# Kernel optimization log

Hardware: AMD Instinct MI355X
Metric: run time of the kernel (lower is better)

The kernel has to match this reference:

```python
import jax, jax.numpy as jnp
import numpy as np

K = 4096
D = 64
DECAY = 0.99
EPS = 1e-05


def setup_inputs() -> dict:
    key = jax.random.key(0)
    k1, k2 = jax.random.split(key)
    z_e = jax.random.normal(k1, (32, 1024, D), dtype=jnp.float32)
    emb = jax.random.normal(k2, (K, D), dtype=jnp.float32)
    emb = emb / jnp.clip(jnp.linalg.norm(emb, axis=1, keepdims=True), 1e-8)
    return {
        "z_e": z_e,
        "embedding": emb,
        "ema_cluster_size": jnp.zeros((K,), jnp.float32),
        "ema_embedding": jnp.zeros((K, D), jnp.float32),
    }


def reference(z_e, embedding, ema_cluster_size, ema_embedding):
    B, L, Dd = z_e.shape
    flat = z_e.reshape(-1, Dd)                                   # (N, D)
    flat_norm = flat / jnp.clip(jnp.linalg.norm(flat, axis=1, keepdims=True), 1e-8)
    dots = flat_norm @ embedding.T                               # (N, K)
    indices = jnp.argmax(dots, axis=1)                           # (N,)
    z_q = embedding[indices].reshape(B, L, Dd)
    z_q_st = z_e + jax.lax.stop_gradient(z_q - z_e)

    # ---- usage / stats ----
    usage = jnp.zeros((K,), jnp.float32).at[indices].add(1.0)    # bincount
    probs = usage / jnp.maximum(usage.sum(), 1.0)
    safe = jnp.where(probs > 0, probs, 1.0)
    perplexity = jnp.exp(-jnp.sum(probs * jnp.log(safe)))
    dead_ratio = jnp.mean((usage == 0).astype(jnp.float32))
    stats = jnp.stack([perplexity, dead_ratio])

    # ---- EMA update (training-mode buffer math, functional) ----
    fn = jax.lax.stop_gradient(flat_norm)
    embed_sum = jnp.zeros((K, Dd), jnp.float32).at[indices].add(fn)  # one_hot.T @ flat_norm
    new_cs = DECAY * ema_cluster_size + (1.0 - DECAY) * usage
    new_ema_emb = DECAY * ema_embedding + (1.0 - DECAY) * embed_sum
    n = new_cs.sum()
    smoothed = (new_cs + EPS) / (n + K * EPS)
    norm_e = new_ema_emb / jnp.clip(smoothed, EPS)[:, None]
    norm_e = norm_e / jnp.clip(jnp.linalg.norm(norm_e, axis=1, keepdims=True), 1e-8)

    # ---- dead-code reinit (reinit_prob=1.0, threshold=0); deterministic key ----
    N = fn.shape[0]
    rand_idx = jax.random.randint(jax.random.key(1), (K,), 0, N)
    src = fn[rand_idx]
    src = src / jnp.clip(jnp.linalg.norm(src, axis=1, keepdims=True), 1e-8)
    dead = usage <= 0.0
    new_embedding = jnp.where(dead[:, None], src, norm_e)

    return (z_q_st, z_q, indices.reshape(B, L), stats,
            new_embedding, new_cs, new_ema_emb)
```

## Files before the change

kernel.cpp:

```cpp
#include <hip/hip_runtime.h>
#include <math.h>

#define N_TOK 32768
#define KCB   4096
#define SPLITS 6

#define OFF_ZQST   0
#define OFF_ZQ     2097152
#define OFF_IDX    4194304
#define OFF_STATS  4227072
#define OFF_NEWEMB 4227074
#define OFF_NEWCS  4489218
#define OFF_NEWEMA 4493314

#define WS_FN       0
#define WS_ESUM     8388608
#define WS_USAGE    9437184
#define WS_CNTS     9453568
#define WS_FULLKEY  9454592
#define WS_EHI      9716736
#define WS_ELO      10241024
#define WS_PK1      10765312
#define WS_PK2      11551744
#define WS_IDXW     12338176
#define WS_RIDX     12469248
#define WS_FULL     12485632
#define WS_FNHI     12616704
#define WS_FNLO     16811008

#define THRKEY 131072u
#define DGRKEY 98304u

typedef __attribute__((ext_vector_type(8))) short short8;
typedef __attribute__((ext_vector_type(4))) short short4v;
typedef __attribute__((ext_vector_type(4))) float float4v;
typedef __attribute__((ext_vector_type(4))) int int4v;

__device__ __forceinline__ float wave_sum(float v) {
#pragma unroll
  for (int off = 32; off > 0; off >>= 1) v += __shfl_xor(v, off, 64);
  return v;
}

__device__ __forceinline__ unsigned short f2bf(float f) {
  unsigned u = __float_as_uint(f);
  unsigned r = (u + 0x7fffu + ((u >> 16) & 1u)) >> 16;
  return (unsigned short)r;
}
__device__ __forceinline__ float bf2f(unsigned short h) {
  return __uint_as_float(((unsigned)h) << 16);
}

typedef const __attribute__((address_space(1))) unsigned int* gas_ptr;
typedef __attribute__((address_space(3))) unsigned int* las_ptr;
__device__ __forceinline__ void gl_lds16(const void* g, void* l) {
  __builtin_amdgcn_global_load_lds((gas_ptr)g, (las_ptr)l, 16, 0, 0);
}

__device__ __forceinline__ unsigned med3u(unsigned a, unsigned b, unsigned c) {
  unsigned r;
  asm("v_med3_u32 %0, %1, %2, %3" : "=v"(r) : "v"(a), "v"(b), "v"(c));
  return r;
}

__device__ __forceinline__ unsigned rotl32(unsigned x, int d) {
  return (x << d) | (x >> (32 - d));
}
__device__ __forceinline__ void tf2x32(unsigned k0, unsigned k1,
                                       unsigned x0, unsigned x1,
                                       unsigned& o0, unsigned& o1) {
  unsigned ks2 = k0 ^ k1 ^ 0x1BD11BDAu;
  unsigned v0 = x0 + k0, v1 = x1 + k1;
  v0 += v1; v1 = rotl32(v1, 13) ^ v0;
  v0 += v1; v1 = rotl32(v1, 15) ^ v0;
  v0 += v1; v1 = rotl32(v1, 26) ^ v0;
  v0 += v1; v1 = rotl32(v1, 6) ^ v0;
  v0 += k1; v1 += ks2 + 1u;
  v0 += v1; v1 = rotl32(v1, 17) ^ v0;
  v0 += v1; v1 = rotl32(v1, 29) ^ v0;
  v0 += v1; v1 = rotl32(v1, 16) ^ v0;
  v0 += v1; v1 = rotl32(v1, 24) ^ v0;
  v0 += ks2; v1 += k0 + 2u;
  v0 += v1; v1 = rotl32(v1, 13) ^ v0;
  v0 += v1; v1 = rotl32(v1, 15) ^ v0;
  v0 += v1; v1 = rotl32(v1, 26) ^ v0;
  v0 += v1; v1 = rotl32(v1, 6) ^ v0;
  v0 += k0; v1 += k1 + 3u;
  v0 += v1; v1 = rotl32(v1, 17) ^ v0;
  v0 += v1; v1 = rotl32(v1, 29) ^ v0;
  v0 += v1; v1 = rotl32(v1, 16) ^ v0;
  v0 += v1; v1 = rotl32(v1, 24) ^ v0;
  v0 += k1; v1 += ks2 + 4u;
  v0 += v1; v1 = rotl32(v1, 13) ^ v0;
  v0 += v1; v1 = rotl32(v1, 15) ^ v0;
  v0 += v1; v1 = rotl32(v1, 26) ^ v0;
  v0 += v1; v1 = rotl32(v1, 6) ^ v0;
  v0 += ks2; v1 += k0 + 5u;
  o0 = v0; o1 = v1;
}

__global__ __launch_bounds__(256) void k_prep(const float* __restrict__ z_e,
                                              const float* __restrict__ emb,
                                              const float* __restrict__ ema_cs,
                                              float* __restrict__ fn,
                                              unsigned short* __restrict__ fnhi,
                                              unsigned short* __restrict__ fnlo,
                                              unsigned short* __restrict__ ehi,
                                              unsigned short* __restrict__ elo,
                                              int* __restrict__ ridx,
                                              int* __restrict__ zbase,
                                              float* __restrict__ scal) {
  __shared__ float rC[4];
  int b = blockIdx.x;
  int t = threadIdx.x;
  if (b < 2048) {
    int wave = t >> 6, lane = t & 63;
    int grp = lane >> 4, l = lane & 15;
    int n = b * 16 + wave * 4 + grp;
    float4v v = ((const float4v*)(z_e + n * 64))[l];
    float4v p;
#pragma unroll
    for (int j = 0; j < 4; j++) p[j] = v[j] * v[j];
#pragma unroll
    for (int j = 0; j < 4; j++) p[j] += __shfl_xor(p[j], 8, 64);
#pragma unroll
    for (int j = 0; j < 4; j++) p[j] += __shfl_xor(p[j], 4, 64);
#pragma unroll
    for (int j = 0; j < 4; j++) p[j] += __shfl_xor(p[j], 2, 64);
#pragma unroll
    for (int j = 0; j < 4; j++) p[j] += __shfl_xor(p[j], 1, 64);
    float t0 = p[0] + p[2], t1 = p[1] + p[3];
    float ss = t0 + t1;
    float d = fmaxf(sqrtf(ss), 1e-8f);
    float4v o;
#pragma unroll
    for (int j = 0; j < 4; j++) o[j] = v[j] / d;
    ((float4v*)(fn + n * 64))[l] = o;
    short4v fh, fl2;
#pragma unroll
    for (int j = 0; j < 4; j++) {
      float f = o[j] * 0.25f;
      unsigned short hu = f2bf(f);
      fh[j] = (short)hu;
      fl2[j] = (short)f2bf(f - bf2f(hu));
    }
    ((short4v*)(fnhi + n * 64))[l] = fh;
    ((short4v*)(fnlo + n * 64))[l] = fl2;
  } else if (b < 2304) {
    int i = (b - 2048) * 1024 + t * 4;
    float4v x = *(const float4v*)(emb + i);
    short4v hh, ll;
#pragma unroll
    for (int j = 0; j < 4; j++) {
      unsigned short hu = f2bf(x[j]);
      hh[j] = (short)hu;
      ll[j] = (short)f2bf(x[j] - bf2f(hu));
    }
    *(short4v*)(ehi + i) = hh;
    *(short4v*)(elo + i) = ll;
  } else if (b < 2312) {
    int j = (b - 2304) * 256 + t;
    unsigned a0, b0, a1, b1;
    tf2x32(0u, 1u, 0u, 2u, a0, b0);
    tf2x32(0u, 1u, 1u, 3u, a1, b1);
    unsigned o0, o1;
    tf2x32(b0, b1, (unsigned)j, (unsigned)(j + 2048), o0, o1);
    ridx[j] = (int)(o0 & 32767u);
    ridx[j + 2048] = (int)(o1 & 32767u);
  } else {
    int i4 = (b - 2312) * 256 + t;
    if (i4 < 66624) ((int4v*)zbase)[i4] = (int4v){0, 0, 0, 0};
    if (b == 2572) {
      __syncthreads();
      float s = 0.f;
#pragma unroll
      for (int j = 0; j < 16; j++) s += ema_cs[j * 256 + t];
      s = wave_sum(s);
      int w = t >> 6, lane = t & 63;
      if (lane == 0) rC[w] = s;
      __syncthreads();
      if (t == 0) scal[2] = 0.99f * (rC[0] + rC[1] + rC[2] + rC[3]) + 327.68f;
    }
  }
}

__global__ __launch_bounds__(256, 3) void k_dots(const unsigned short* __restrict__ fnhi,
                                                 const unsigned short* __restrict__ fnlo,
                                                 const unsigned short* __restrict__ ehi,
                                                 const unsigned short* __restrict__ elo,
                                                 unsigned* __restrict__ pk1,
                                                 unsigned* __restrict__ pk2) {
  __shared__ unsigned short lds_b[2][2][2][1024];
  int t = threadIdx.x;
  int wave = t >> 6, lane = t & 63;
  int g = lane >> 4, n = lane & 15;
  int qw = blockIdx.x * 256 + wave * 64;
  int split = blockIdx.y;
  int nt16 = (split < 2) ? 704 : 672;
  int tstart16 = (split < 3) ? 704 * split : 672 * split + 64;
  int ntiles = nt16 >> 4;
  int npairs = ntiles >> 1;

  short8 ahi[4][2], alo[4][2];
#pragma unroll
  for (int s = 0; s < 4; s++)
#pragma unroll
    for (int ks = 0; ks < 2; ks++) {
      int off = (qw + s * 16 + n) * 64 + ks * 32 + g * 8;
      ahi[s][ks] = *(const short8*)(fnhi + off);
      alo[s][ks] = *(const short8*)(fnlo + off);
    }

  unsigned run1[4][4], run2[4][4];
#pragma unroll
  for (int s = 0; s < 4; s++)
#pragma unroll
    for (int r = 0; r < 4; r++) { run1[s][r] = 0u; run2[s][r] = 0u; }

  const float hiclamp = __uint_as_float(0x3F9FFFFFu);

  int stile = wave >> 1;
  int shl = wave & 1;
  const unsigned short* sbase = shl ? elo : ehi;
  int c0 = lane ^ ((lane >> 3) & 7);

#define STAGE(BUF, PAIR)                                                        \
    {                                                                           \
      const unsigned short* sg =                                                \
          sbase + (tstart16 + ((PAIR) * 2 + stile) * 16) * 64;                  \
      gl_lds16(sg + c0 * 8, &lds_b[BUF][stile][shl][0]);                        \
      gl_lds16(sg + 512 + c0 * 8, &lds_b[BUF][stile][shl][512]);                \
    }

  int sh0 = (n * 8 + (g ^ (n & 7))) * 8;
  int sh1 = (n * 8 + ((g + 4) ^ (n & 7))) * 8;

#define MFMA_BLOCK(H0, H1, L0, L1)                                              \
    float4v a0 = (float4v){1.125f, 1.125f, 1.125f, 1.125f};                     \
    float4v a1 = a0, a2 = a0, a3 = a0;                                          \
    a0 = __builtin_amdgcn_mfma_f32_16x16x32_bf16(alo[0][0], H0, a0, 0, 0, 0);   \
    a1 = __builtin_amdgcn_mfma_f32_16x16x32_bf16(alo[1][0], H0, a1, 0, 0, 0);   \
    a2 = __builtin_amdgcn_mfma_f32_16x16x32_bf16(alo[2][0], H0, a2, 0, 0, 0);   \
    a3 = __builtin_amdgcn_mfma_f32_16x16x32_bf16(alo[3][0], H0, a3, 0, 0, 0);   \
    a0 = __builtin_amdgcn_mfma_f32_16x16x32_bf16(alo[0][1], H1, a0, 0, 0, 0);   \
    a1 = __builtin_amdgcn_mfma_f32_16x16x32_bf16(alo[1][1], H1, a1, 0, 0, 0);   \
    a2 = __builtin_amdgcn_mfma_f32_16x16x32_bf16(alo[2][1], H1, a2, 0, 0, 0);   \
    a3 = __builtin_amdgcn_mfma_f32_16x16x32_bf16(alo[3][1], H1, a3, 0, 0, 0);   \
    a0 = __builtin_amdgcn_mfma_f32_16x16x32_bf16(ahi[0][0], L0, a0, 0, 0, 0);   \
    a1 = __builtin_amdgcn_mfma_f32_16x16x32_bf16(ahi[1][0], L0, a1, 0, 0, 0);   \
    a2 = __builtin_amdgcn_mfma_f32_16x16x32_bf16(ahi[2][0], L0, a2, 0, 0, 0);   \
    a3 = __builtin_amdgcn_mfma_f32_16x16x32_bf16(ahi[3][0], L0, a3, 0, 0, 0);   \
    a0 = __builtin_amdgcn_mfma_f32_16x16x32_bf16(ahi[0][1], L1, a0, 0, 0, 0);   \
    a1 = __builtin_amdgcn_mfma_f32_16x16x32_bf16(ahi[1][1], L1, a1, 0, 0, 0);   \
    a2 = __builtin_amdgcn_mfma_f32_16x16x32_bf16(ahi[2][1], L1, a2, 0, 0, 0);   \
    a3 = __builtin_amdgcn_mfma_f32_16x16x32_bf16(ahi[3][1], L1, a3, 0, 0, 0);   \
    a0 = __builtin_amdgcn_mfma_f32_16x16x32_bf16(ahi[0][0], H0, a0, 0, 0, 0);   \
    a1 = __builtin_amdgcn_mfma_f32_16x16x32_bf16(ahi[1][0], H0, a1, 0, 0, 0);   \
    a2 = __builtin_amdgcn_mfma_f32_16x16x32_bf16(ahi[2][0], H0, a2, 0, 0, 0);   \
    a3 = __builtin_amdgcn_mfma_f32_16x16x32_bf16(ahi[3][0], H0, a3, 0, 0, 0);   \
    a0 = __builtin_amdgcn_mfma_f32_16x16x32_bf16(ahi[0][1], H1, a0, 0, 0, 0);   \
    a1 = __builtin_amdgcn_mfma_f32_16x16x32_bf16(ahi[1][1], H1, a1, 0, 0, 0);   \
    a2 = __builtin_amdgcn_mfma_f32_16x16x32_bf16(ahi[2][1], H1, a2, 0, 0, 0);   \
    a3 = __builtin_amdgcn_mfma_f32_16x16x32_bf16(ahi[3][1], H1, a3, 0, 0, 0);

#define SELECT_BLOCK(KT)                                                        \
    {                                                                           \
      unsigned invb = (unsigned)(nt16 - 1 - (KT) * 16 - n);                     \
      _Pragma("unroll") for (int r = 0; r < 4; r++) {                           \
        float x0 = __builtin_amdgcn_fmed3f(a0[r], 1.0f, hiclamp);               \
        unsigned kb0 = (__float_as_uint(x0) << 10) + invb;                      \
        run2[0][r] = med3u(run1[0][r], run2[0][r], kb0);                        \
        run1[0][r] = max(run1[0][r], kb0);                                      \
        float x1 = __builtin_amdgcn_fmed3f(a1[r], 1.0f, hiclamp);               \
        unsigned kb1 = (__float_as_uint(x1) << 10) + invb;                      \
        run2[1][r] = med3u(run1[1][r], run2[1][r], kb1);                        \
        run1[1][r] = max(run1[1][r], kb1);                                      \
        float x2 = __builtin_amdgcn_fmed3f(a2[r], 1.0f, hiclamp);               \
        unsigned kb2 = (__float_as_uint(x2) << 10) + invb;                      \
        run2[2][r] = med3u(run1[2][r], run2[2][r], kb2);                        \
        run1[2][r] = max(run1[2][r], kb2);                                      \
        float x3 = __builtin_amdgcn_fmed3f(a3[r], 1.0f, hiclamp);               \
        unsigned kb3 = (__float_as_uint(x3) << 10) + invb;                      \
        run2[3][r] = med3u(run1[3][r], run2[3][r], kb3);                        \
        run1[3][r] = max(run1[3][r], kb3);                                      \
      }                                                                         \
    }

  STAGE(0, 0)
  __syncthreads();
  int bb = 0;
#pragma unroll 1
  for (int p = 0; p < npairs; p++) {
    if (p + 1 < npairs) STAGE(bb ^ 1, p + 1)
    {
      short8 H0 = *(const short8*)&lds_b[bb][0][0][sh0];
      short8 H1 = *(const short8*)&lds_b[bb][0][0][sh1];
      short8 L0 = *(const short8*)&lds_b[bb][0][1][sh0];
      short8 L1 = *(const short8*)&lds_b[bb][0][1][sh1];
      MFMA_BLOCK(H0, H1, L0, L1)
      SELECT_BLOCK(p * 2)
    }
    {
      short8 H0 = *(const short8*)&lds_b[bb][1][0][sh0];
      short8 H1 = *(const short8*)&lds_b[bb][1][0][sh1];
      short8 L0 = *(const short8*)&lds_b[bb][1][1][sh0];
      short8 L1 = *(const short8*)&lds_b[bb][1][1][sh1];
      MFMA_BLOCK(H0, H1, L0, L1)
      SELECT_BLOCK(p * 2 + 1)
    }
    __syncthreads();
    bb ^= 1;
  }
#undef MFMA_BLOCK
#undef SELECT_BLOCK
#undef STAGE

#pragma unroll
  for (int off = 1; off <= 8; off <<= 1) {
#pragma unroll
    for (int s = 0; s < 4; s++)
#pragma unroll
      for (int r = 0; r < 4; r++) {
        unsigned o1 = (unsigned)__shfl_xor((int)run1[s][r], off, 64);
        unsigned o2 = (unsigned)__shfl_xor((int)run2[s][r], off, 64);
        run2[s][r] = max(min(run1[s][r], o1), max(run2[s][r], o2));
        run1[s][r] = max(run1[s][r], o1);
      }
  }

  if (n == 0) {
#pragma unroll
    for (int s = 0; s < 4; s++)
#pragma unroll
      for (int r = 0; r < 4; r++) {
        int q = qw + s * 16 + g * 4 + r;
        pk1[split * N_TOK + q] = run1[s][r];
        pk2[split * N_TOK + q] = run2[s][r];
      }
  }
}

__global__ __launch_bounds__(256) void k_merge_fix(const unsigned* __restrict__ pk1,
                                                   const unsigned* __restrict__ pk2,
                                                   const float* __restrict__ fn,
                                                   const float* __restrict__ emb,
                                                   int* __restrict__ idxw,
                                                   int* __restrict__ cnts,
                                                   int* __restrict__ full,
                                                   unsigned long long* __restrict__ fullkey) {
  __shared__ int nfl;
  __shared__ int fl[256][13];
  int t = threadIdx.x;
  if (t == 0) nfl = 0;
  __syncthreads();
  int q = blockIdx.x * 256 + t;
  unsigned k1v[SPLITS], k2v[SPLITS];
  unsigned b1 = 0u, b2 = 0u;
  int s1 = 0;
#pragma unroll
  for (int s = 0; s < SPLITS; s++) {
    unsigned k1 = pk1[s * N_TOK + q];
    unsigned k2 = pk2[s * N_TOK + q];
    k1v[s] = k1;
    k2v[s] = k2;
    b2 = max(b2, min(b1, k1));
    b2 = max(b2, k2);
    if (k1 > b1) { b1 = k1; s1 = s; }
  }
  int nt16s = (s1 < 2) ? 704 : 672;
  int ts16 = (s1 < 3) ? 704 * s1 : 672 * s1 + 64;
  idxw[q] = ts16 + nt16s - 1 - (int)(b1 & 1023u);
  fullkey[q] = 0ull;
  bool danger = false;
#pragma unroll
  for (int s = 0; s < SPLITS; s++) danger |= (k2v[s] + DGRKEY > b1);
  if (danger) {
    int p = atomicAdd(&cnts[0], 1);
    full[p] = q;
  } else if (b1 - b2 < THRKEY) {
    int p = atomicAdd(&nfl, 1);
    fl[p][0] = q;
#pragma unroll
    for (int s = 0; s < SPLITS; s++) {
      int nt = (s < 2) ? 704 : 672;
      int tss = (s < 3) ? 704 * s : 672 * s + 64;
      fl[p][1 + s] = tss + nt - 1 - (int)(k1v[s] & 1023u);
      fl[p][7 + s] = tss + nt - 1 - (int)(k2v[s] & 1023u);
    }
  }
  __syncthreads();
  int m = nfl;
  int wave = t >> 6, lane = t & 63;
  int c = lane >> 2, dg = lane & 3;
  for (int i = wave; i < m; i += 4) {
    int fq = fl[i][0];
    int code = (c < 12) ? fl[i][1 + c] : fl[i][1];
    const float* er = emb + code * 64 + dg * 16;
    const float* fr = fn + fq * 64 + dg * 16;
    double d = 0.0;
#pragma unroll
    for (int k = 0; k < 16; k++) d += (double)er[k] * (double)fr[k];
    d += __shfl_xor(d, 1, 64);
    d += __shfl_xor(d, 2, 64);
    unsigned long long key =
        ((unsigned long long)__double_as_longlong(d + 2.0) & ~0xFFFULL) |
        (unsigned long long)(4095 - code);
    if (c >= 12) key = 0ull;
#pragma unroll
    for (int off = 4; off <= 32; off <<= 1) {
      unsigned long long o = __shfl_xor(key, off, 64);
      key = key > o ? key : o;
    }
    if (lane == 0) idxw[fq] = 4095 - (int)(key & 0xFFFULL);
  }
}

__global__ __launch_bounds__(256) void k_fix_full(const int* __restrict__ cnts,
                                                  const int* __restrict__ full,
                                                  const float* __restrict__ fn,
                                                  const float* __restrict__ emb,
                                                  unsigned long long* __restrict__ fullkey) {
  __shared__ float sfn[64];
  __shared__ unsigned long long red[256];
  int t = threadIdx.x;
  int chunk = blockIdx.x & 15;
  int c = chunk * 256 + t;
  float cr[64];
  {
    const float4v* er4 = (const float4v*)(emb + c * 64);
#pragma unroll
    for (int kk = 0; kk < 16; kk++) {
      float4v v = er4[kk];
      cr[kk * 4 + 0] = v[0];
      cr[kk * 4 + 1] = v[1];
      cr[kk * 4 + 2] = v[2];
      cr[kk * 4 + 3] = v[3];
    }
  }
  int total = cnts[0];
  total = total < N_TOK ? total : N_TOK;
  int qstride = (int)(gridDim.x >> 4);
  for (int w = (int)(blockIdx.x >> 4); w < total; w += qstride) {
    int q = full[w];
    __syncthreads();
    if (t < 64) sfn[t] = fn[q * 64 + t];
    __syncthreads();
    double s0 = 0, s1 = 0, s2 = 0, s3 = 0;
#pragma unroll
    for (int k = 0; k < 16; k++) {
      s0 += (double)cr[k] * (double)sfn[k];
      s1 += (double)cr[k + 16] * (double)sfn[k + 16];
      s2 += (double)cr[k + 32] * (double)sfn[k + 32];
      s3 += (double)cr[k + 48] * (double)sfn[k + 48];
    }
    double d = (s0 + s1) + (s2 + s3);
    unsigned long long key =
        ((unsigned long long)__double_as_longlong(d + 2.0) & ~0xFFFULL) |
        (unsigned long long)(4095 - c);
    red[t] = key;
    __syncthreads();
    for (int s = 128; s > 0; s >>= 1) {
      if (t < s) red[t] = red[t] > red[t + s] ? red[t] : red[t + s];
      __syncthreads();
    }
    if (t == 0) atomicMax(&fullkey[q], red[0]);
  }
}

__global__ __launch_bounds__(256) void k_write_scatter(const int* __restrict__ idxw,
                                                       const unsigned long long* __restrict__ fullkey,
                                                       const float* __restrict__ z_e,
                                                       const float* __restrict__ emb,
                                                       const float* __restrict__ fn,
                                                       float* __restrict__ out,
                                                       float* __restrict__ esum,
                                                       float* __restrict__ usage) {
  int t = threadIdx.x;
  int nn = blockIdx.x * 4 + (t >> 6);
  int lane = t & 63;
  unsigned long long fk = fullkey[nn];
  int bi = fk ? (4095 - (int)(fk & 0xFFFULL)) : idxw[nn];
  float v = emb[bi * 64 + lane];
  float ze = z_e[nn * 64 + lane];
  out[OFF_ZQST + nn * 64 + lane] = ze + (v - ze);
  out[OFF_ZQ + nn * 64 + lane] = v;
  atomicAdd(&esum[bi * 64 + lane], fn[nn * 64 + lane]);
  if (lane == 0) {
    out[OFF_IDX + nn] = (float)bi;
    atomicAdd(&usage[bi], 1.0f);
  }
}

__global__ __launch_bounds__(256) void k_final(const float* __restrict__ usage,
                                               const float* __restrict__ ema_cs,
                                               const float* __restrict__ ema_emb,
                                               const float* __restrict__ esum,
                                               const float* __restrict__ fn,
                                               const int* __restrict__ ridx,
                                               const float* __restrict__ scal,
                                               float* __restrict__ out) {
  int t = threadIdx.x;
  if (blockIdx.x == 1024) {
    __shared__ float rE[4], rD[4];
    float ent = 0.f, dead = 0.f;
#pragma unroll
    for (int j = 0; j < 16; j++) {
      float u = usage[j * 256 + t];
      float p = u * (1.0f / 32768.0f);
      ent += (p > 0.f) ? p * logf(p) : 0.f;
      dead += (u == 0.f) ? 1.f : 0.f;
    }
    ent = wave_sum(ent);
    dead = wave_sum(dead);
    int w = t >> 6, lane = t & 63;
    if (lane == 0) { rE[w] = ent; rD[w] = dead; }
    __syncthreads();
    if (t == 0) {
      out[OFF_STATS + 0] = expf(-(rE[0] + rE[1] + rE[2] + rE[3]));
      out[OFF_STATS + 1] = (rD[0] + rD[1] + rD[2] + rD[3]) * (1.0f / 4096.0f);
    }
    return;
  }
  int k = blockIdx.x * 4 + (t >> 6);
  int lane = t & 63;
  float u = usage[k];
  float ncs = 0.99f * ema_cs[k] + 0.01f * u;
  if (lane == 0) out[OFF_NEWCS + k] = ncs;
  float nee = 0.99f * ema_emb[k * 64 + lane] + 0.01f * esum[k * 64 + lane];
  out[OFF_NEWEMA + k * 64 + lane] = nee;

  float n = scal[2];
  float smoothed = (ncs + 1e-5f) / (n + 4096.0f * 1e-5f);
  float ne = nee / fmaxf(smoothed, 1e-5f);
  float ss = wave_sum(ne * ne);
  ne = ne / fmaxf(sqrtf(ss), 1e-8f);

  float res;
  if (u <= 0.f) {
    int rsrc = ridx[k];
    float v = fn[rsrc * 64 + lane];
    float s2 = wave_sum(v * v);
    res = v / fmaxf(sqrtf(s2), 1e-8f);
  } else {
    res = ne;
  }
  out[OFF_NEWEMB + k * 64 + lane] = res;
}

extern "C" void kernel_launch(void* const* d_in, const int* in_sizes, int n_in,
                              void* d_out, int out_size, void* d_ws, size_t ws_size,
                              hipStream_t stream) {
  const float* z_e = (const float*)d_in[0];
  const float* emb = (const float*)d_in[1];
  const float* ema_cs = (const float*)d_in[2];
  const float* ema_emb = (const float*)d_in[3];
  float* out = (float*)d_out;
  char* ws = (char*)d_ws;

  float* fn = (float*)(ws + WS_FN);
  float* esum = (float*)(ws + WS_ESUM);
  float* usage = (float*)(ws + WS_USAGE);
  int* cnts = (int*)(ws + WS_CNTS);
  float* scal = (float*)(ws + WS_CNTS + 16);
  unsigned long long* fullkey = (unsigned long long*)(ws + WS_FULLKEY);
  unsigned short* ehi = (unsigned short*)(ws + WS_EHI);
  unsigned short* elo = (unsigned short*)(ws + WS_ELO);
  unsigned* pk1 = (unsigned*)(ws + WS_PK1);
  unsigned* pk2 = (unsigned*)(ws + WS_PK2);
  int* idxw = (int*)(ws + WS_IDXW);
  int* ridx = (int*)(ws + WS_RIDX);
  int* full = (int*)(ws + WS_FULL);
  unsigned short* fnhi = (unsigned short*)(ws + WS_FNHI);
  unsigned short* fnlo = (unsigned short*)(ws + WS_FNLO);

  k_prep<<<2573, 256, 0, stream>>>(z_e, emb, ema_cs, fn, fnhi, fnlo, ehi, elo,
                                   ridx, (int*)(ws + WS_ESUM), scal);
  k_dots<<<dim3(128, SPLITS), 256, 0, stream>>>(fnhi, fnlo, ehi, elo, pk1, pk2);
  k_merge_fix<<<128, 256, 0, stream>>>(pk1, pk2, fn, emb, idxw, cnts, full, fullkey);
  k_fix_full<<<1024, 256, 0, stream>>>(cnts, full, fn, emb, fullkey);
  k_write_scatter<<<8192, 256, 0, stream>>>(idxw, fullkey, z_e, emb, fn, out, esum, usage);
  k_final<<<1025, 256, 0, stream>>>(usage, ema_cs, ema_emb, esum, fn, ridx, scal, out);
}
```

Before: 148.3 us.

## Split k_dots codebook range across wave pairs and merge top-2 in LDS

Each block now handles 128 tokens instead of 256. The two wave pairs that share a token group each scan half of the split's codebook tile pairs, using separate double-buffered LDS regions. Their per-token top-2 packed keys are merged through LDS before the write to pk1/pk2. The grid doubles to 256x6 blocks, which raises occupancy and parallelism, at the cost of loading A fragments twice per token, more LDS, and lockstep iterations with idle waves when the halves are uneven.

```diff
diff --git a/kernel.cpp b/kernel.cpp
--- a/kernel.cpp
+++ b/kernel.cpp
@@ -190,16 +190,19 @@
                                                  const unsigned short* __restrict__ elo,
                                                  unsigned* __restrict__ pk1,
                                                  unsigned* __restrict__ pk2) {
-  __shared__ unsigned short lds_b[2][2][2][1024];
+  __shared__ unsigned short lds_b[2][2][2][2][1024];
   int t = threadIdx.x;
   int wave = t >> 6, lane = t & 63;
   int g = lane >> 4, n = lane & 15;
-  int qw = blockIdx.x * 256 + wave * 64;
+  int qg = wave >> 1, half = wave & 1;
+  int qw = blockIdx.x * 128 + qg * 64;
   int split = blockIdx.y;
   int nt16 = (split < 2) ? 704 : 672;
   int tstart16 = (split < 3) ? 704 * split : 672 * split + 64;
   int ntiles = nt16 >> 4;
   int npairs = ntiles >> 1;
+  int p0 = half * 11;
+  int pend = half ? npairs : 11;
 
   short8 ahi[4][2], alo[4][2];
 #pragma unroll
@@ -219,17 +222,20 @@
 
   const float hiclamp = __uint_as_float(0x3F9FFFFFu);
 
-  int stile = wave >> 1;
-  int shl = wave & 1;
+  int shl = qg;
   const unsigned short* sbase = shl ? elo : ehi;
   int c0 = lane ^ ((lane >> 3) & 7);
 
 #define STAGE(BUF, PAIR)                                                        \
     {                                                                           \
-      const unsigned short* sg =                                                \
-          sbase + (tstart16 + ((PAIR) * 2 + stile) * 16) * 64;                  \
-      gl_lds16(sg + c0 * 8, &lds_b[BUF][stile][shl][0]);                        \
-      gl_lds16(sg + 512 + c0 * 8, &lds_b[BUF][stile][shl][512]);                \
+      const unsigned short* sg0 =                                               \
+          sbase + (tstart16 + ((PAIR) * 2 + 0) * 16) * 64;                      \
+      const unsigned short* sg1 =                                               \
+          sbase + (tstart16 + ((PAIR) * 2 + 1) * 16) * 64;                      \
+      gl_lds16(sg0 + c0 * 8, &lds_b[half][BUF][0][shl][0]);                     \
+      gl_lds16(sg0 + 512 + c0 * 8, &lds_b[half][BUF][0][shl][512]);             \
+      gl_lds16(sg1 + c0 * 8, &lds_b[half][BUF][1][shl][0]);                     \
+      gl_lds16(sg1 + 512 + c0 * 8, &lds_b[half][BUF][1][shl][512]);             \
     }
 
   int sh0 = (n * 8 + (g ^ (n & 7))) * 8;
@@ -286,27 +292,31 @@
       }                                                                         \
     }
 
-  STAGE(0, 0)
+  STAGE(0, p0)
   __syncthreads();
   int bb = 0;
 #pragma unroll 1
-  for (int p = 0; p < npairs; p++) {
-    if (p + 1 < npairs) STAGE(bb ^ 1, p + 1)
-    {
-      short8 H0 = *(const short8*)&lds_b[bb][0][0][sh0];
-      short8 H1 = *(const short8*)&lds_b[bb][0][0][sh1];
-      short8 L0 = *(const short8*)&lds_b[bb][0][1][sh0];
-      short8 L1 = *(const short8*)&lds_b[bb][0][1][sh1];
-      MFMA_BLOCK(H0, H1, L0, L1)
-      SELECT_BLOCK(p * 2)
-    }
-    {
-      short8 H0 = *(const short8*)&lds_b[bb][1][0][sh0];
-      short8 H1 = *(const short8*)&lds_b[bb][1][0][sh1];
-      short8 L0 = *(const short8*)&lds_b[bb][1][1][sh0];
-      short8 L1 = *(const short8*)&lds_b[bb][1][1][sh1];
-      MFMA_BLOCK(H0, H1, L0, L1)
-      SELECT_BLOCK(p * 2 + 1)
+  for (int pr = 0; pr < 11; pr++) {
+    int pair = p0 + pr;
+    bool act = pair < pend;
+    if (act && pair + 1 < pend) STAGE(bb ^ 1, pair + 1)
+    if (act) {
+      {
+        short8 H0 = *(const short8*)&lds_b[half][bb][0][0][sh0];
+        short8 H1 = *(const short8*)&lds_b[half][bb][0][0][sh1];
+        short8 L0 = *(const short8*)&lds_b[half][bb][0][1][sh0];
+        short8 L1 = *(const short8*)&lds_b[half][bb][0][1][sh1];
+        MFMA_BLOCK(H0, H1, L0, L1)
+        SELECT_BLOCK(pair * 2)
+      }
+      {
+        short8 H0 = *(const short8*)&lds_b[half][bb][1][0][sh0];
+        short8 H1 = *(const short8*)&lds_b[half][bb][1][0][sh1];
+        short8 L0 = *(const short8*)&lds_b[half][bb][1][1][sh0];
+        short8 L1 = *(const short8*)&lds_b[half][bb][1][1][sh1];
+        MFMA_BLOCK(H0, H1, L0, L1)
+        SELECT_BLOCK(pair * 2 + 1)
+      }
     }
     __syncthreads();
     bb ^= 1;
@@ -328,15 +338,29 @@
       }
   }
 
+  unsigned* mb = (unsigned*)lds_b;
   if (n == 0) {
 #pragma unroll
     for (int s = 0; s < 4; s++)
 #pragma unroll
       for (int r = 0; r < 4; r++) {
-        int q = qw + s * 16 + g * 4 + r;
-        pk1[split * N_TOK + q] = run1[s][r];
-        pk2[split * N_TOK + q] = run2[s][r];
+        int ql = s * 16 + g * 4 + r;
+        mb[wave * 64 + ql] = run1[s][r];
+        mb[256 + wave * 64 + ql] = run2[s][r];
       }
+  }
+  __syncthreads();
+  if (t < 128) {
+    int qg2 = t >> 6, ql = t & 63;
+    unsigned k1a = mb[(qg2 * 2 + 0) * 64 + ql];
+    unsigned k1b = mb[(qg2 * 2 + 1) * 64 + ql];
+    unsigned k2a = mb[256 + (qg2 * 2 + 0) * 64 + ql];
+    unsigned k2b = mb[256 + (qg2 * 2 + 1) * 64 + ql];
+    unsigned b1 = max(k1a, k1b);
+    unsigned b2 = max(min(k1a, k1b), max(k2a, k2b));
+    int q = blockIdx.x * 128 + qg2 * 64 + ql;
+    pk1[split * N_TOK + q] = b1;
+    pk2[split * N_TOK + q] = b2;
   }
 }
 
@@ -575,7 +599,7 @@
 
   k_prep<<<2573, 256, 0, stream>>>(z_e, emb, ema_cs, fn, fnhi, fnlo, ehi, elo,
                                    ridx, (int*)(ws + WS_ESUM), scal);
-  k_dots<<<dim3(128, SPLITS), 256, 0, stream>>>(fnhi, fnlo, ehi, elo, pk1, pk2);
+  k_dots<<<dim3(256, SPLITS), 256, 0, stream>>>(fnhi, fnlo, ehi, elo, pk1, pk2);
   k_merge_fix<<<128, 256, 0, stream>>>(pk1, pk2, fn, emb, idxw, cnts, full, fullkey);
   k_fix_full<<<1024, 256, 0, stream>>>(cnts, full, fn, emb, fullkey);
   k_write_scatter<<<8192, 256, 0, stream>>>(idxw, fullkey, z_e, emb, fn, out, esum, usage);
```

Result: slower. 154.3 us (+4.0%).
